# Kernel optimization log

Measured on AMD Instinct MI355X. Metric: run time of the kernel, lower is better.

## Reference

```python
import jax, jax.numpy as jnp
import numpy as np

N_USER = 20000
N_ITEM = 20000
N = N_USER + N_ITEM          # total nodes
D = 128                      # n_hid (= in_feats = out_feats)
H = 4                        # GAT heads
L = 2                        # n_layers
M = 8                        # mem_size (hypernet bottleneck)
T = 5                        # num_rels in MemoryLayer
E_UI = 40000                 # user->item bipartite edges
E_T = 16000                  # homogeneous edges per relation type (grouped)
EPS = 1e-5


def _layer_norm(x, w, b):
    mu = x.mean(-1, keepdims=True)
    var = ((x - mu) ** 2).mean(-1, keepdims=True)
    return (x - mu) * jax.lax.rsqrt(var + EPS) * w + b


def _gat(h_src, h_dst, src_idx, dst_idx, n_dst, W, al, ar, bias):
    """DGL GATConv (shared fc, eval-mode dropout=identity, elu activation)."""
    fs = (h_src @ W.T).reshape(-1, H, D)          # [Ns, H, D]
    fd = (h_dst @ W.T).reshape(-1, H, D)          # [Nd, H, D]
    el = (fs * al).sum(-1)                        # [Ns, H]
    er = (fd * ar).sum(-1)                        # [Nd, H]
    e = jax.nn.leaky_relu(el[src_idx] + er[dst_idx], 0.2)   # [E, H]
    emax = jax.ops.segment_max(e, dst_idx, num_segments=n_dst)
    ex = jnp.exp(e - emax[dst_idx])
    denom = jax.ops.segment_sum(ex, dst_idx, num_segments=n_dst)
    a = ex / denom[dst_idx]                       # edge softmax per dst
    rst = jax.ops.segment_sum(a[:, :, None] * fs[src_idx], dst_idx, num_segments=n_dst)
    return jax.nn.elu(rst + bias.reshape(1, H, D))           # [Nd, H, D]


def _memory_layer(feat, edge_src, edge_dst, Wc, bc, Ww, nWc, nbc, nWw, h_bias, ln_w, ln_b):
    # edges grouped by relation type: edge_src/edge_dst are [T, E_T]
    hs = feat[edge_src]                           # [T, Et, D]
    hd = feat[edge_dst]                           # [T, Et, D]
    # per-edge hypernetwork: coef = LeakyReLU(Linear(dst)); w = Ww(coef); msg = w @ src
    coef = jax.nn.leaky_relu(jnp.einsum('ted,tmd->tem', hd, Wc) + bc[:, None, :], 0.2)
    tmp = jnp.einsum('tei,tmoi->temo', hs, Ww)    # [T, Et, M, D] -- M-bottleneck path
    msg = jnp.einsum('tem,temo->teo', coef, tmp)  # [T, Et, D]
    flat_dst = edge_dst.reshape(-1)
    s = jax.ops.segment_sum(msg.reshape(-1, D), flat_dst, num_segments=N)
    cnt = jax.ops.segment_sum(jnp.ones((flat_dst.shape[0],), feat.dtype), flat_dst, num_segments=N)
    agg = s / jnp.maximum(cnt, 1.0)[:, None]      # fn.mean (0 for isolated nodes)
    rep = _layer_norm(agg, ln_w, ln_b) + h_bias
    # self-loop node_ME(feat, feat)
    ncoef = jax.nn.leaky_relu(feat @ nWc.T + nbc, 0.2)       # [N, M]
    ntmp = jnp.einsum('ni,moi->nmo', feat, nWw)              # [N, M, D]
    rep = rep + jnp.einsum('nm,nmo->no', ncoef, ntmp)
    return jax.nn.leaky_relu(rep, 0.2)            # dropout = identity (eval)


def setup_inputs() -> dict:
    key = jax.random.key(0)
    ks = jax.random.split(key, 16)
    s = 0.05
    return {
        "embedding": jax.random.normal(ks[0], (N, D), jnp.float32),
        "gat_fc_W": jax.random.normal(ks[1], (L, 2, H * D, D), jnp.float32) * s,
        "gat_attn_l": jax.random.normal(ks[2], (L, 2, H, D), jnp.float32) * s,
        "gat_attn_r": jax.random.normal(ks[3], (L, 2, H, D), jnp.float32) * s,
        "gat_bias": jnp.zeros((L, 2, H * D), jnp.float32),
        "proj_W": jax.random.normal(ks[4], (L, 2, D, H * D), jnp.float32) * s,
        "proj_b": jnp.zeros((L, 2, D), jnp.float32),
        "mem_rel_Wc": jax.random.normal(ks[5], (L, T, M, D), jnp.float32) * s,
        "mem_rel_bc": jnp.zeros((L, T, M), jnp.float32),
        "mem_rel_Ww": jax.random.normal(ks[6], (L, T, M, D, D), jnp.float32) * s,
        "mem_node_Wc": jax.random.normal(ks[7], (L, M, D), jnp.float32) * s,
        "mem_node_bc": jnp.zeros((L, M), jnp.float32),
        "mem_node_Ww": jax.random.normal(ks[8], (L, M, D, D), jnp.float32) * s,
        "mem_h_bias": jnp.zeros((L, D), jnp.float32),
        "mem_ln_w": jnp.ones((L, D), jnp.float32),
        "mem_ln_b": jnp.zeros((L, D), jnp.float32),
        "final_ln_w": jnp.ones(((L + 1) * D,), jnp.float32),
        "final_ln_b": jnp.zeros(((L + 1) * D,), jnp.float32),
        "src_u": jax.random.randint(ks[9], (E_UI,), 0, N_USER, jnp.int32),
        "dst_i": jax.random.randint(ks[10], (E_UI,), 0, N_ITEM, jnp.int32),
        "edge_src": jax.random.randint(ks[11], (T, E_T), 0, N, jnp.int32),
        "edge_dst": jax.random.randint(ks[12], (T, E_T), 0, N, jnp.int32),
    }


def reference(embedding, gat_fc_W, gat_attn_l, gat_attn_r, gat_bias, proj_W, proj_b,
              mem_rel_Wc, mem_rel_bc, mem_rel_Ww, mem_node_Wc, mem_node_bc, mem_node_Ww,
              mem_h_bias, mem_ln_w, mem_ln_b, final_ln_w, final_ln_b,
              src_u, dst_i, edge_src, edge_dst):
    features = embedding
    all_emb = [features]
    for l in range(L):
        hu, hi = features[:N_USER], features[N_USER:]
        # relation 0: item -> user (dst = user)
        gu = _gat(hi, hu, dst_i, src_u, N_USER,
                  gat_fc_W[l, 0], gat_attn_l[l, 0], gat_attn_r[l, 0], gat_bias[l, 0])
        ru = jax.nn.elu(gu.reshape(N_USER, H * D) @ proj_W[l, 0].T + proj_b[l, 0])
        # relation 1: user -> item (dst = item)
        gi = _gat(hu, hi, src_u, dst_i, N_ITEM,
                  gat_fc_W[l, 1], gat_attn_l[l, 1], gat_attn_r[l, 1], gat_bias[l, 1])
        ri = jnp.asarray(jax.nn.elu(gi.reshape(N_ITEM, H * D) @ proj_W[l, 1].T + proj_b[l, 1]))
        trans = jnp.concatenate([ru, ri], axis=0)             # [N, D]
        mem = _memory_layer(all_emb[-1], edge_src, edge_dst,
                            mem_rel_Wc[l], mem_rel_bc[l], mem_rel_Ww[l],
                            mem_node_Wc[l], mem_node_bc[l], mem_node_Ww[l],
                            mem_h_bias[l], mem_ln_w[l], mem_ln_b[l])
        features = mem + trans
        all_emb.append(features)
    return _layer_norm(jnp.concatenate(all_emb, axis=1), final_ln_w, final_ln_b)
```

## Files before the change

### kernel.cpp

```cpp
#include <hip/hip_runtime.h>
#include <hip/hip_bf16.h>
#include <math.h>

typedef __hip_bfloat16 bf16;

#define NUSER 20000
#define NITEM 20000
#define NTOT  40000
#define DD    128
#define HH    4
#define TT    5
#define MMEM  8
#define EUI   40000
#define ET    16000

#define MP_N  40064
#define MP_H  20096

typedef __attribute__((ext_vector_type(8))) short short8;
typedef __attribute__((ext_vector_type(4))) float f32x4;

__device__ __forceinline__ void gload16(const bf16* g, bf16* l){
  __builtin_amdgcn_global_load_lds(
      (const __attribute__((address_space(1))) unsigned int*)g,
      (__attribute__((address_space(3))) unsigned int*)l, 16, 0, 0);
}

__device__ __forceinline__ int stage_cg(int lane){
  return (((lane&3) ^ ((lane>>2)&3) ^ (lane>>4)) << 3);
}
__device__ __forceinline__ int read_pc8(int lm, int lq){
  return ((lq ^ (lm&3) ^ ((lm>>2)&3)) << 3);
}

__global__ __launch_bounds__(256) void k_mfma_gemm(
    const bf16* __restrict__ A, const bf16* __restrict__ B,
    const float* __restrict__ bias, float* __restrict__ C,
    long Astr, long Bstr, long biasStr, long Cstr,
    int ldc, int M, int K, int act, int accum)
{
  A += (size_t)blockIdx.z*Astr; B += (size_t)blockIdx.z*Bstr;
  if (bias) bias += (size_t)blockIdx.z*biasStr;
  C += (size_t)blockIdx.z*Cstr;
  __shared__ bf16 As[128*32];
  __shared__ bf16 Bs[128*32];
  int tid = threadIdx.x;
  int wave = tid >> 6, lane = tid & 63;
  int r0 = blockIdx.x * 128, c0 = blockIdx.y * 128;
  int wm = (wave >> 1) * 64, wn = (wave & 1) * 64;
  f32x4 acc[4][4];
  #pragma unroll
  for (int i=0;i<4;i++)
    #pragma unroll
    for (int j=0;j<4;j++) acc[i][j] = (f32x4){0.f,0.f,0.f,0.f};

  int rq = lane >> 2;
  int cg = stage_cg(lane);
  const bf16* Ag = A + (size_t)(r0 + wave*32 + rq)*K + cg;
  const bf16* Bg = B + (size_t)(c0 + wave*32 + rq)*K + cg;
  bf16* AsW = As + wave*32*32;
  bf16* BsW = Bs + wave*32*32;
  int lm = lane & 15, lq = lane >> 4;
  int pc8 = read_pc8(lm, lq);
  const bf16* Ard = As + (wm + lm)*32 + pc8;
  const bf16* Brd = Bs + (wn + lm)*32 + pc8;

  for (int k0 = 0; k0 < K; k0 += 32){
    gload16(Ag + k0,            AsW);
    gload16(Ag + 16*K + k0,     AsW + 16*32);
    gload16(Bg + k0,            BsW);
    gload16(Bg + 16*K + k0,     BsW + 16*32);
    __syncthreads();
    short8 af[4], bfv[4];
    #pragma unroll
    for (int i=0;i<4;i++) af[i]  = *(const short8*)(Ard + i*16*32);
    #pragma unroll
    for (int j=0;j<4;j++) bfv[j] = *(const short8*)(Brd + j*16*32);
    #pragma unroll
    for (int i=0;i<4;i++)
      #pragma unroll
      for (int j=0;j<4;j++)
        acc[i][j] = __builtin_amdgcn_mfma_f32_16x16x32_bf16(af[i], bfv[j], acc[i][j], 0, 0, 0);
    __syncthreads();
  }
  #pragma unroll
  for (int i=0;i<4;i++){
    #pragma unroll
    for (int j=0;j<4;j++){
      int c = c0 + wn + j*16 + lm;
      #pragma unroll
      for (int rg=0; rg<4; rg++){
        int r = r0 + wm + i*16 + lq*4 + rg;
        if (r < M){
          float v = acc[i][j][rg];
          if (bias) v += bias[c];
          if (act==1) v = v>0.f ? v : expm1f(v);
          float* cp = &C[(size_t)r*ldc + c];
          if (accum) *cp += v; else *cp = v;
        }
      }
    }
  }
}

__global__ __launch_bounds__(256) void k_memgemm(
    const float* __restrict__ feat, const int* __restrict__ src,
    const float* __restrict__ coef, const bf16* __restrict__ B,
    float* __restrict__ C,
    long srcStr, long coefStr, long Bstr, long Cstr,
    int Mvalid, int accum)
{
  __shared__ bf16 Af[128*136];
  __shared__ float cfS[128*8];
  __shared__ bf16 Bs[2][128*32];
  int t = blockIdx.y;
  const int*   srcT  = src ? src + (size_t)t*srcStr : nullptr;
  const float* coefT = coef + (size_t)t*coefStr;
  const bf16*  Bt    = B + (size_t)t*Bstr;
  float*       Ct    = C + (size_t)t*Cstr;
  int tid = threadIdx.x, wave = tid >> 6, lane = tid & 63;
  int r0 = blockIdx.x * 128;

  {
    int rL = tid >> 1, hf = tid & 1;
    int r = r0 + rL;
    bool valid = r < Mvalid;
    int s = valid ? (srcT ? srcT[r] : r) : 0;
    const float4* fp = (const float4*)(feat + (size_t)s*128 + hf*64);
    bf16* ap = Af + rL*136 + hf*64;
    #pragma unroll
    for (int q=0;q<16;q++){
      float4 v = fp[q];
      __hip_bfloat162 p0 = __float22bfloat162_rn(make_float2(v.x, v.y));
      __hip_bfloat162 p1 = __float22bfloat162_rn(make_float2(v.z, v.w));
      *(__hip_bfloat162*)(ap + q*4)     = p0;
      *(__hip_bfloat162*)(ap + q*4 + 2) = p1;
    }
    if (hf == 0){
      float4 c0v, c1v;
      if (valid){
        c0v = *(const float4*)(coefT + (size_t)r*8);
        c1v = *(const float4*)(coefT + (size_t)r*8 + 4);
      } else { c0v = make_float4(0.f,0.f,0.f,0.f); c1v = c0v; }
      *(float4*)(cfS + rL*8)     = c0v;
      *(float4*)(cfS + rL*8 + 4) = c1v;
    }
  }

  int rq = lane >> 2;
  int cg = stage_cg(lane);
  const bf16* Bg0 = Bt + (size_t)(wave*32 + rq)*1024 + cg;
  const bf16* Bg1 = Bt + (size_t)(wave*32 + 16 + rq)*1024 + cg;

  int wm = (wave >> 1) * 64, wn = (wave & 1) * 64;
  int lm = lane & 15, lq = lane >> 4;
  int pc8 = read_pc8(lm, lq);

  f32x4 acc[4][4];
  #pragma unroll
  for (int i=0;i<4;i++)
    #pragma unroll
    for (int j=0;j<4;j++) acc[i][j] = (f32x4){0.f,0.f,0.f,0.f};

  {
    bf16* d = Bs[0] + wave*1024;
    gload16(Bg0, d);
    gload16(Bg1, d + 512);
  }
  __syncthreads();

  int buf = 0;
  for (int m = 0; m < 8; m++){
    float cfr[4];
    #pragma unroll
    for (int i=0;i<4;i++) cfr[i] = cfS[(wm + i*16 + lm)*8 + m];
    #pragma unroll
    for (int ic = 0; ic < 4; ic++){
      int kk = m*4 + ic;
      if (kk + 1 < 32){
        int k1 = (kk + 1) * 32;
        bf16* d = Bs[buf^1] + wave*1024;
        gload16(Bg0 + k1, d);
        gload16(Bg1 + k1, d + 512);
      }
      short8 af[4], bfv[4];
      #pragma unroll
      for (int i=0;i<4;i++){
        short8 raw = *(const short8*)(Af + (size_t)(wm + i*16 + lm)*136 + ic*32 + lq*8);
        union { short8 s; unsigned u[4]; } U, V;
        U.s = raw;
        float c = cfr[i];
        #pragma unroll
        for (int p=0;p<4;p++){
          float lo = __uint_as_float(U.u[p] << 16) * c;
          float hi = __uint_as_float(U.u[p] & 0xffff0000u) * c;
          __hip_bfloat162 pk = __float22bfloat162_rn(make_float2(lo, hi));
          V.u[p] = *(unsigned*)&pk;
        }
        af[i] = V.s;
      }
      #pragma unroll
      for (int j=0;j<4;j++)
        bfv[j] = *(const short8*)(Bs[buf] + (wn + lm + j*16)*32 + pc8);
      #pragma unroll
      for (int i=0;i<4;i++)
        #pragma unroll
        for (int j=0;j<4;j++)
          acc[i][j] = __builtin_amdgcn_mfma_f32_16x16x32_bf16(af[i], bfv[j], acc[i][j], 0, 0, 0);
      __syncthreads();
      buf ^= 1;
    }
  }
  #pragma unroll
  for (int i=0;i<4;i++){
    #pragma unroll
    for (int j=0;j<4;j++){
      int c = wn + j*16 + lm;
      #pragma unroll
      for (int rg=0; rg<4; rg++){
        int r = r0 + wm + i*16 + lq*4 + rg;
        if (r < Mvalid){
          float* cp = &Ct[(size_t)r*128 + c];
          if (accum) *cp += acc[i][j][rg]; else *cp = acc[i][j][rg];
        }
      }
    }
  }
}

__global__ void k_f2b(const float* __restrict__ in, bf16* __restrict__ o, int nv, int nt){
  int i = blockIdx.x*256 + threadIdx.x;
  if (i < nt) o[i] = __float2bfloat16(i < nv ? in[i] : 0.f);
}

__global__ void k_repack(const float* __restrict__ in, bf16* __restrict__ o){
  int s = blockIdx.y;
  int g = blockIdx.x*256 + threadIdx.x;
  int m = g >> 14, od = (g >> 7) & 127, i = g & 127;
  o[(size_t)s*131072 + (size_t)od*1024 + m*128 + i] = __float2bfloat16(in[(size_t)s*131072 + g]);
}

__global__ void k_rstb(const float* __restrict__ rst, const float* __restrict__ gb,
                       bf16* __restrict__ o){
  int r = blockIdx.x, t = threadIdx.x;
  int k = t*4;
  bf16* op = o + (size_t)r*512 + k;
  if (r < 20000){
    const float* ip = rst + (size_t)r*512 + k;
    #pragma unroll
    for (int q=0;q<4;q++){
      float v = ip[q] + gb[k+q];
      v = v>0.f ? v : expm1f(v);
      op[q] = __float2bfloat16(v);
    }
  } else {
    #pragma unroll
    for (int q=0;q<4;q++) op[q] = __float2bfloat16(0.f);
  }
}

__global__ void k_attn(const float* __restrict__ F, const float* __restrict__ al,
                       const float* __restrict__ ar, float* __restrict__ el, float* __restrict__ er){
  int n = blockIdx.x, lane = threadIdx.x;
  const float* row = F + (size_t)n*512;
  #pragma unroll
  for (int h=0;h<HH;h++){
    float x1 = row[h*128+lane], x2 = row[h*128+64+lane];
    float vl = x1*al[h*128+lane] + x2*al[h*128+64+lane];
    float vr = x1*ar[h*128+lane] + x2*ar[h*128+64+lane];
    #pragma unroll
    for (int off=32;off;off>>=1){ vl += __shfl_xor(vl,off); vr += __shfl_xor(vr,off); }
    if (lane==0){ el[n*4+h]=vl; er[n*4+h]=vr; }
  }
}

__global__ void k_hist(const int* __restrict__ dIdx, int* __restrict__ cnt, int E){
  int e = blockIdx.x*256+threadIdx.x;
  if (e<E) atomicAdd(&cnt[dIdx[e]], 1);
}

__global__ __launch_bounds__(1024) void k_scan(const int* __restrict__ in,
                                               int* __restrict__ out, int n){
  __shared__ int wsum[16];
  __shared__ int carry;
  int tidx = threadIdx.x, lane = tidx & 63, w = tidx >> 6;
  if (tidx == 0) carry = 0;
  __syncthreads();
  for (int base = 0; base < n; base += 1024){
    int i = base + tidx;
    int v = (i < n) ? in[i] : 0;
    int x = v;
    #pragma unroll
    for (int off = 1; off < 64; off <<= 1){
      int t = __shfl_up(x, off);
      if (lane >= off) x += t;
    }
    if (lane == 63) wsum[w] = x;
    __syncthreads();
    if (w == 0 && lane < 16){
      int t = wsum[lane];
      #pragma unroll
      for (int off=1; off<16; off<<=1){
        int u = __shfl_up(t, off, 16);
        if (lane >= off) t += u;
      }
      wsum[lane] = t;
    }
    __syncthreads();
    int woff = (w == 0) ? 0 : wsum[w-1];
    int excl = carry + woff + x - v;
    if (i < n) out[i] = excl;
    __syncthreads();
    if (tidx == 1023) carry = carry + wsum[15];
    __syncthreads();
  }
  if (tidx == 0) out[n] = carry;
}

__global__ void k_csr_scatter(const int* __restrict__ sIdx, const int* __restrict__ dIdx,
                              int sOff, const int* __restrict__ rowptr,
                              int* __restrict__ cursor, int* __restrict__ col, int E){
  int e = blockIdx.x*256+threadIdx.x; if (e>=E) return;
  int d = dIdx[e];
  int pos = rowptr[d] + atomicAdd(&cursor[d], 1);
  col[pos] = sIdx[e] + sOff;
}

__global__ void k_csr_scatter_eid(const int* __restrict__ dIdx, const int* __restrict__ rowptr,
                                  int* __restrict__ cursor, int* __restrict__ col, int E){
  int e = blockIdx.x*256+threadIdx.x; if (e>=E) return;
  int d = dIdx[e];
  int pos = rowptr[d] + atomicAdd(&cursor[d], 1);
  col[pos] = e;
}

__global__ __launch_bounds__(64) void k_gat_gather(
    const int* __restrict__ rowptr, const int* __restrict__ col,
    const float* __restrict__ el, const float* __restrict__ er,
    const float* __restrict__ F, float* __restrict__ rst,
    int dOff, int n_dst)
{
  int dl = blockIdx.x;
  int dn = dl + dOff;
  int lane = threadIdx.x;
  int h = lane >> 4;
  int off = (lane & 15) << 3;
  float erh = er[dn*4 + h];
  float m = -INFINITY, den = 0.f;
  float acc[8];
  #pragma unroll
  for (int i=0;i<8;i++) acc[i]=0.f;
  int jb = rowptr[dl], je = rowptr[dl+1];
  for (int j=jb; j<je; j++){
    int s = col[j];
    float e = el[s*4+h] + erh;
    e = e > 0.f ? e : 0.2f*e;
    float mn = fmaxf(m, e);
    float sc = __expf(m - mn);
    float wj = __expf(e - mn);
    den = den*sc + wj;
    m = mn;
    const float4* fp = (const float4*)(F + (size_t)s*512 + h*128 + off);
    float4 f0 = fp[0], f1 = fp[1];
    acc[0]=acc[0]*sc + wj*f0.x; acc[1]=acc[1]*sc + wj*f0.y;
    acc[2]=acc[2]*sc + wj*f0.z; acc[3]=acc[3]*sc + wj*f0.w;
    acc[4]=acc[4]*sc + wj*f1.x; acc[5]=acc[5]*sc + wj*f1.y;
    acc[6]=acc[6]*sc + wj*f1.z; acc[7]=acc[7]*sc + wj*f1.w;
  }
  float inv = den > 0.f ? 1.f/den : 0.f;
  float* rp = rst + (size_t)dl*512 + h*128 + off;
  ((float4*)rp)[0] = make_float4(acc[0]*inv, acc[1]*inv, acc[2]*inv, acc[3]*inv);
  ((float4*)rp)[1] = make_float4(acc[4]*inv, acc[5]*inv, acc[6]*inv, acc[7]*inv);
}

__global__ void k_coef(const float* __restrict__ feat, const int* __restrict__ idx,
                       const float* __restrict__ Wc, const float* __restrict__ bc,
                       float* __restrict__ outc, int cnt){
  int t = blockIdx.y;
  __shared__ float wS[MMEM*DD];
  __shared__ float bS[MMEM];
  for (int i=threadIdx.x;i<MMEM*DD;i+=128) wS[i] = Wc[(size_t)t*MMEM*DD + i];
  if (threadIdx.x < MMEM) bS[threadIdx.x] = bc[t*MMEM + threadIdx.x];
  __syncthreads();
  int e = blockIdx.x*128 + threadIdx.x; if (e >= cnt) return;
  int node = idx ? idx[(size_t)t*cnt + e] : e;
  float acc[MMEM];
  #pragma unroll
  for (int m=0;m<MMEM;m++) acc[m]=bS[m];
  const float* fr = feat + (size_t)node*DD;
  for (int d2=0; d2<DD; d2++){
    float v = fr[d2];
    #pragma unroll
    for (int m=0;m<MMEM;m++) acc[m] = fmaf(v, wS[m*DD+d2], acc[m]);
  }
  float* op = outc + ((size_t)t*cnt + e)*MMEM;
  #pragma unroll
  for (int m=0;m<MMEM;m++){ float v=acc[m]; op[m] = v>0.f ? v : 0.2f*v; }
}

__global__ void k_mem_gather(const int* __restrict__ rpT, const int* __restrict__ colT,
                             const float* __restrict__ msg, float* __restrict__ sAgg){
  int n = blockIdx.x*4 + (threadIdx.x >> 6);
  if (n >= NTOT) return;
  int lane = threadIdx.x & 63;
  int jb = rpT[n], je = rpT[n+1];
  float a0=0.f, a1=0.f;
  for (int j=jb;j<je;j++){
    const float* mp = msg + (size_t)colT[j]*128;
    a0 += mp[lane]; a1 += mp[lane+64];
  }
  sAgg[(size_t)n*128+lane] = a0;
  sAgg[(size_t)n*128+64+lane] = a1;
}

__global__ void k_memln(const float* __restrict__ s, const int* __restrict__ rpT,
                        const float* __restrict__ lw, const float* __restrict__ lb,
                        const float* __restrict__ hb, float* __restrict__ outp){
  int n = blockIdx.x, lane = threadIdx.x;
  float c = fmaxf((float)(rpT[n+1]-rpT[n]), 1.f);
  float x1 = s[(size_t)n*128+lane]/c, x2 = s[(size_t)n*128+64+lane]/c;
  float t = x1+x2;
  #pragma unroll
  for (int off=32;off;off>>=1) t += __shfl_xor(t,off);
  float mu = t * (1.f/128.f);
  float d1=x1-mu, d2=x2-mu;
  float v = d1*d1+d2*d2;
  #pragma unroll
  for (int off=32;off;off>>=1) v += __shfl_xor(v,off);
  float r = rsqrtf(v*(1.f/128.f) + 1e-5f);
  outp[(size_t)n*128+lane]    = d1*r*lw[lane]    + lb[lane]    + hb[lane];
  outp[(size_t)n*128+64+lane] = d2*r*lw[64+lane] + lb[64+lane] + hb[64+lane];
}

__global__ void k_final_feat(const float* __restrict__ mo, const float* __restrict__ tr,
                             float* __restrict__ o, int n){
  int i = blockIdx.x*256+threadIdx.x; if (i>=n) return;
  float v = mo[i]; v = v>0.f ? v : 0.2f*v;
  o[i] = v + tr[i];
}

__global__ void k_final_ln(const float* __restrict__ emb, const float* __restrict__ f1,
                           const float* __restrict__ f2, const float* __restrict__ w,
                           const float* __restrict__ b, float* __restrict__ out){
  int n = blockIdx.x, t = threadIdx.x;
  __shared__ float red[4];
  float x0 = emb[(size_t)n*128+t];
  float x1 = f1[(size_t)n*128+t];
  float x2 = f2[(size_t)n*128+t];
  float s = x0+x1+x2;
  #pragma unroll
  for (int off=32;off;off>>=1) s += __shfl_xor(s,off);
  if ((t&63)==0) red[t>>6] = s;
  __syncthreads();
  float mu = (red[0]+red[1]) * (1.f/384.f);
  float d0=x0-mu, d1=x1-mu, d2=x2-mu;
  float v = d0*d0+d1*d1+d2*d2;
  #pragma unroll
  for (int off=32;off;off>>=1) v += __shfl_xor(v,off);
  if ((t&63)==0) red[2+(t>>6)] = v;
  __syncthreads();
  float var = (red[2]+red[3]) * (1.f/384.f);
  float r = rsqrtf(var + 1e-5f);
  size_t o = (size_t)n*384;
  out[o+t]     = d0*r*w[t]     + b[t];
  out[o+128+t] = d1*r*w[128+t] + b[128+t];
  out[o+256+t] = d2*r*w[256+t] + b[256+t];
}

extern "C" void kernel_launch(void* const* d_in, const int* in_sizes, int n_in,
                              void* d_out, int out_size, void* d_ws, size_t ws_size,
                              hipStream_t stream)
{
  const float* emb   = (const float*)d_in[0];
  const float* fcW   = (const float*)d_in[1];
  const float* attl  = (const float*)d_in[2];
  const float* attr  = (const float*)d_in[3];
  const float* gbias = (const float*)d_in[4];
  const float* projW = (const float*)d_in[5];
  const float* projB = (const float*)d_in[6];
  const float* relWc = (const float*)d_in[7];
  const float* relbc = (const float*)d_in[8];
  const float* relWw = (const float*)d_in[9];
  const float* nodWc = (const float*)d_in[10];
  const float* nodbc = (const float*)d_in[11];
  const float* nodWw = (const float*)d_in[12];
  const float* hbias = (const float*)d_in[13];
  const float* mlnw  = (const float*)d_in[14];
  const float* mlnb  = (const float*)d_in[15];
  const float* flnw  = (const float*)d_in[16];
  const float* flnb  = (const float*)d_in[17];
  const int*  srcU  = (const int*)d_in[18];
  const int*  dstI  = (const int*)d_in[19];
  const int*  eSrc  = (const int*)d_in[20];
  const int*  eDst  = (const int*)d_in[21];
  float* out = (float*)d_out;

  char* wp = (char*)d_ws;
  auto alloc = [&](size_t bytes)->void* {
    void* p = (void*)wp; wp += (bytes + 511) & ~(size_t)511; return p;
  };
  float* feat1 = (float*)alloc((size_t)NTOT*DD*4);
  float* feat2 = (float*)alloc((size_t)NTOT*DD*4);
  float* Fbuf  = (float*)alloc((size_t)NTOT*512*4);
  float* rst   = (float*)alloc((size_t)(NTOT+256)*512*4);
  float* trans = (float*)alloc((size_t)NTOT*DD*4);
  float* elF   = (float*)alloc((size_t)NTOT*4*4);
  float* erF   = (float*)alloc((size_t)NTOT*4*4);
  int* rpA  = (int*)alloc((size_t)(NUSER+1)*4);
  int* colA = (int*)alloc((size_t)EUI*4);
  int* rpB  = (int*)alloc((size_t)(NITEM+1)*4);
  int* colB = (int*)alloc((size_t)EUI*4);
  int* icnt = (int*)alloc((size_t)20000*4);
  int* icur = (int*)alloc((size_t)20000*4);
  int* rpT  = (int*)alloc((size_t)(NTOT+1)*4);
  int* colT = (int*)alloc((size_t)TT*ET*4);
  int* cntT = (int*)alloc((size_t)NTOT*4);
  int* icurT= (int*)alloc((size_t)NTOT*4);
  bf16* featb  = (bf16*)alloc((size_t)MP_N*DD*2);
  bf16* fcWb   = (bf16*)alloc((size_t)4*512*DD*2);
  bf16* projWb = (bf16*)alloc((size_t)4*DD*512*2);
  bf16* relWwb = (bf16*)alloc((size_t)10*DD*1024*2);
  bf16* nodWwb = (bf16*)alloc((size_t)2*DD*1024*2);
  bf16* rstb0 = (bf16*)(rst + (size_t)20000*512);
  bf16* rstb1 = rstb0 + (size_t)MP_H*512;
  float* sAgg   = rst;
  float* memO   = rst + (size_t)NTOT*DD;
  float* msgB   = Fbuf;
  float* coefB  = Fbuf + (size_t)TT*ET*128;
  float* ncoefB = coefB + (size_t)TT*ET*8;

  k_f2b<<<dim3((4*512*DD+255)/256),256,0,stream>>>(fcW, fcWb, 4*512*DD, 4*512*DD);
  k_f2b<<<dim3((4*DD*512+255)/256),256,0,stream>>>(projW, projWb, 4*DD*512, 4*DD*512);
  k_repack<<<dim3(512,10),256,0,stream>>>(relWw, relWwb);
  k_repack<<<dim3(512,2),256,0,stream>>>(nodWw, nodWwb);

  hipMemsetAsync(icnt, 0, 20000*4, stream);
  hipMemsetAsync(icur, 0, 20000*4, stream);
  k_hist<<<dim3((EUI+255)/256),256,0,stream>>>(srcU, icnt, EUI);
  k_scan<<<dim3(1),1024,0,stream>>>(icnt, rpA, NUSER);
  k_csr_scatter<<<dim3((EUI+255)/256),256,0,stream>>>(dstI, srcU, NUSER, rpA, icur, colA, EUI);
  hipMemsetAsync(icnt, 0, 20000*4, stream);
  hipMemsetAsync(icur, 0, 20000*4, stream);
  k_hist<<<dim3((EUI+255)/256),256,0,stream>>>(dstI, icnt, EUI);
  k_scan<<<dim3(1),1024,0,stream>>>(icnt, rpB, NITEM);
  k_csr_scatter<<<dim3((EUI+255)/256),256,0,stream>>>(srcU, dstI, 0, rpB, icur, colB, EUI);
  hipMemsetAsync(cntT, 0, NTOT*4, stream);
  hipMemsetAsync(icurT, 0, NTOT*4, stream);
  k_hist<<<dim3((TT*ET+255)/256),256,0,stream>>>(eDst, cntT, TT*ET);
  k_scan<<<dim3(1),1024,0,stream>>>(cntT, rpT, NTOT);
  k_csr_scatter_eid<<<dim3((TT*ET+255)/256),256,0,stream>>>(eDst, rpT, icurT, colT, TT*ET);

  const float* feats[3] = {emb, feat1, feat2};
  for (int l=0; l<2; l++){
    const float* fin  = feats[l];
    float* fout = (float*)feats[l+1];

    k_f2b<<<dim3((MP_N*DD+255)/256),256,0,stream>>>(fin, featb, NTOT*DD, MP_N*DD);

    for (int d=0; d<2; d++){
      k_mfma_gemm<<<dim3(MP_N/128, 4, 1),256,0,stream>>>(
          featb, fcWb + (size_t)(l*2+d)*512*DD, nullptr, Fbuf,
          0,0,0,0, 512, NTOT, DD, 0, 0);
      k_attn<<<dim3(NTOT),64,0,stream>>>(Fbuf,
          attl+(size_t)(l*2+d)*512, attr+(size_t)(l*2+d)*512, elF, erF);
      int dOff = (d==0) ? 0 : NUSER;
      const int* rp  = (d==0) ? rpA : rpB;
      const int* col = (d==0) ? colA : colB;
      k_gat_gather<<<dim3(20000),64,0,stream>>>(rp, col, elF, erF, Fbuf, rst, dOff, 20000);
      k_rstb<<<dim3(MP_H),128,0,stream>>>(rst, gbias+(size_t)(l*2+d)*512,
                                          (d==0) ? rstb0 : rstb1);
    }
    k_mfma_gemm<<<dim3(MP_H/128, 1, 2),256,0,stream>>>(
        rstb0, projWb + (size_t)(l*2)*DD*512, projB + (size_t)(l*2)*DD, trans,
        (long)MP_H*512, (long)DD*512, (long)DD, (long)20000*DD,
        DD, 20000, 512, 1, 0);

    k_coef<<<dim3((ET+127)/128, TT),128,0,stream>>>(fin, eDst,
        relWc+(size_t)l*TT*MMEM*DD, relbc+(size_t)l*TT*MMEM, coefB, ET);
    k_memgemm<<<dim3(ET/128, TT),256,0,stream>>>(
        fin, eSrc, coefB, relWwb + (size_t)l*TT*DD*1024, msgB,
        (long)ET, (long)ET*8, (long)DD*1024, (long)ET*128, ET, 0);
    k_mem_gather<<<dim3(NTOT/4),256,0,stream>>>(rpT, colT, msgB, sAgg);
    k_memln<<<dim3(NTOT),64,0,stream>>>(sAgg, rpT, mlnw+(size_t)l*DD, mlnb+(size_t)l*DD,
                                        hbias+(size_t)l*DD, memO);
    k_coef<<<dim3((NTOT+127)/128, 1),128,0,stream>>>(fin, nullptr,
        nodWc+(size_t)l*MMEM*DD, nodbc+(size_t)l*MMEM, ncoefB, NTOT);
    k_memgemm<<<dim3(MP_N/128, 1),256,0,stream>>>(
        fin, nullptr, ncoefB, nodWwb + (size_t)l*DD*1024, memO,
        0, 0, 0, 0, NTOT, 1);
    k_final_feat<<<dim3((NTOT*DD+255)/256),256,0,stream>>>(memO, trans, fout, NTOT*DD);
  }

  k_final_ln<<<dim3(NTOT),128,0,stream>>>(emb, feat1, feat2, flnw, flnb, out);
}
```

Measured before the change: 1.053 ms.

## Fuse attention scores into FC GEMM, store bf16 intermediates, restructure memgemm

```diff
diff --git a/kernel.cpp b/kernel.cpp
--- a/kernel.cpp
+++ b/kernel.cpp
@@ -25,6 +25,8 @@
       (const __attribute__((address_space(1))) unsigned int*)g,
       (__attribute__((address_space(3))) unsigned int*)l, 16, 0, 0);
 }
+__device__ __forceinline__ float bu2f_lo(unsigned u){ return __uint_as_float(u << 16); }
+__device__ __forceinline__ float bu2f_hi(unsigned u){ return __uint_as_float(u & 0xffff0000u); }
 
 __device__ __forceinline__ int stage_cg(int lane){
   return (((lane&3) ^ ((lane>>2)&3) ^ (lane>>4)) << 3);
@@ -103,48 +105,151 @@
   }
 }
 
+__global__ __launch_bounds__(256) void k_fc_gemm(
+    const bf16* __restrict__ A, const bf16* __restrict__ B,
+    bf16* __restrict__ Fb, const float* __restrict__ al, const float* __restrict__ ar,
+    float* __restrict__ el, float* __restrict__ er, int M)
+{
+  __shared__ bf16 As[128*32];
+  __shared__ bf16 Bs[128*32];
+  __shared__ float redE[2][2][128];
+  int tid = threadIdx.x;
+  int wave = tid >> 6, lane = tid & 63;
+  int h = blockIdx.y;
+  int r0 = blockIdx.x * 128;
+  int wm = (wave >> 1) * 64, wn = (wave & 1) * 64;
+  f32x4 acc[4][4];
+  #pragma unroll
+  for (int i=0;i<4;i++)
+    #pragma unroll
+    for (int j=0;j<4;j++) acc[i][j] = (f32x4){0.f,0.f,0.f,0.f};
+
+  int rq = lane >> 2;
+  int cg = stage_cg(lane);
+  const bf16* Ag = A + (size_t)(r0 + wave*32 + rq)*128 + cg;
+  const bf16* Bg = B + (size_t)(h*128 + wave*32 + rq)*128 + cg;
+  bf16* AsW = As + wave*32*32;
+  bf16* BsW = Bs + wave*32*32;
+  int lm = lane & 15, lq = lane >> 4;
+  int pc8 = read_pc8(lm, lq);
+  const bf16* Ard = As + (wm + lm)*32 + pc8;
+  const bf16* Brd = Bs + (wn + lm)*32 + pc8;
+
+  for (int k0 = 0; k0 < 128; k0 += 32){
+    gload16(Ag + k0,             AsW);
+    gload16(Ag + 16*128 + k0,    AsW + 16*32);
+    gload16(Bg + k0,             BsW);
+    gload16(Bg + 16*128 + k0,    BsW + 16*32);
+    __syncthreads();
+    short8 af[4], bfv[4];
+    #pragma unroll
+    for (int i=0;i<4;i++) af[i]  = *(const short8*)(Ard + i*16*32);
+    #pragma unroll
+    for (int j=0;j<4;j++) bfv[j] = *(const short8*)(Brd + j*16*32);
+    #pragma unroll
+    for (int i=0;i<4;i++)
+      #pragma unroll
+      for (int j=0;j<4;j++)
+        acc[i][j] = __builtin_amdgcn_mfma_f32_16x16x32_bf16(af[i], bfv[j], acc[i][j], 0, 0, 0);
+    __syncthreads();
+  }
+  float alv[4], arv[4];
+  #pragma unroll
+  for (int j=0;j<4;j++){
+    int c = h*128 + wn + j*16 + lm;
+    alv[j] = al[c]; arv[j] = ar[c];
+  }
+  int wnh = wave & 1;
+  #pragma unroll
+  for (int i=0;i<4;i++){
+    #pragma unroll
+    for (int rg=0; rg<4; rg++){
+      float se = 0.f, sr = 0.f;
+      #pragma unroll
+      for (int j=0;j<4;j++){
+        float v = acc[i][j][rg];
+        se = fmaf(v, alv[j], se);
+        sr = fmaf(v, arv[j], sr);
+      }
+      #pragma unroll
+      for (int msk=1; msk<16; msk<<=1){
+        se += __shfl_xor(se, msk);
+        sr += __shfl_xor(sr, msk);
+      }
+      if (lm == 0){
+        int rl = wm + i*16 + lq*4 + rg;
+        redE[0][wnh][rl] = se;
+        redE[1][wnh][rl] = sr;
+      }
+    }
+  }
+  #pragma unroll
+  for (int i=0;i<4;i++){
+    #pragma unroll
+    for (int j=0;j<4;j++){
+      int c = h*128 + wn + j*16 + lm;
+      #pragma unroll
+      for (int rg=0; rg<4; rg++){
+        int r = r0 + wm + i*16 + lq*4 + rg;
+        if (r < M) Fb[(size_t)r*512 + c] = __float2bfloat16(acc[i][j][rg]);
+      }
+    }
+  }
+  __syncthreads();
+  if (tid < 128){
+    int r = r0 + tid;
+    if (r < M) el[(size_t)r*4 + h] = redE[0][0][tid] + redE[0][1][tid];
+  } else {
+    int t2 = tid - 128;
+    int r = r0 + t2;
+    if (r < M) er[(size_t)r*4 + h] = redE[1][0][t2] + redE[1][1][t2];
+  }
+}
+
 __global__ __launch_bounds__(256) void k_memgemm(
     const float* __restrict__ feat, const int* __restrict__ src,
     const float* __restrict__ coef, const bf16* __restrict__ B,
-    float* __restrict__ C,
-    long srcStr, long coefStr, long Bstr, long Cstr,
-    int Mvalid, int accum)
+    float* __restrict__ C, bf16* __restrict__ Cb,
+    const float* __restrict__ trans, float* __restrict__ fout,
+    long srcStr, long coefStr, long Bstr, long CbStr,
+    int Mvalid, int mode)
 {
-  __shared__ bf16 Af[128*136];
-  __shared__ float cfS[128*8];
+  __shared__ bf16 Af[64*144];
+  __shared__ float cfS[8*64];
   __shared__ bf16 Bs[2][128*32];
   int t = blockIdx.y;
   const int*   srcT  = src ? src + (size_t)t*srcStr : nullptr;
   const float* coefT = coef + (size_t)t*coefStr;
   const bf16*  Bt    = B + (size_t)t*Bstr;
-  float*       Ct    = C + (size_t)t*Cstr;
   int tid = threadIdx.x, wave = tid >> 6, lane = tid & 63;
-  int r0 = blockIdx.x * 128;
+  int r0 = blockIdx.x * 64;
 
   {
-    int rL = tid >> 1, hf = tid & 1;
+    int rL = tid >> 2, seg = tid & 3;
     int r = r0 + rL;
     bool valid = r < Mvalid;
     int s = valid ? (srcT ? srcT[r] : r) : 0;
-    const float4* fp = (const float4*)(feat + (size_t)s*128 + hf*64);
-    bf16* ap = Af + rL*136 + hf*64;
-    #pragma unroll
-    for (int q=0;q<16;q++){
-      float4 v = fp[q];
-      __hip_bfloat162 p0 = __float22bfloat162_rn(make_float2(v.x, v.y));
-      __hip_bfloat162 p1 = __float22bfloat162_rn(make_float2(v.z, v.w));
+    const float4* fp = (const float4*)(feat + (size_t)s*128 + seg*32);
+    bf16* ap = Af + rL*144 + seg*32;
+    #pragma unroll
+    for (int q=0;q<8;q+=2){
+      float4 v0 = fp[q], v1 = fp[q+1];
+      __hip_bfloat162 p0 = __float22bfloat162_rn(make_float2(v0.x, v0.y));
+      __hip_bfloat162 p1 = __float22bfloat162_rn(make_float2(v0.z, v0.w));
+      __hip_bfloat162 p2 = __float22bfloat162_rn(make_float2(v1.x, v1.y));
+      __hip_bfloat162 p3 = __float22bfloat162_rn(make_float2(v1.z, v1.w));
       *(__hip_bfloat162*)(ap + q*4)     = p0;
       *(__hip_bfloat162*)(ap + q*4 + 2) = p1;
-    }
-    if (hf == 0){
-      float4 c0v, c1v;
-      if (valid){
-        c0v = *(const float4*)(coefT + (size_t)r*8);
-        c1v = *(const float4*)(coefT + (size_t)r*8 + 4);
-      } else { c0v = make_float4(0.f,0.f,0.f,0.f); c1v = c0v; }
-      *(float4*)(cfS + rL*8)     = c0v;
-      *(float4*)(cfS + rL*8 + 4) = c1v;
-    }
+      *(__hip_bfloat162*)(ap + q*4 + 4) = p2;
+      *(__hip_bfloat162*)(ap + q*4 + 6) = p3;
+    }
+  }
+  if (tid < 64){
+    int r = r0 + tid;
+    bool valid = r < Mvalid;
+    #pragma unroll
+    for (int m=0;m<8;m++)
+      cfS[m*64 + tid] = valid ? coefT[(size_t)r*8 + m] : 0.f;
   }
 
   int rq = lane >> 2;
@@ -152,15 +257,15 @@
   const bf16* Bg0 = Bt + (size_t)(wave*32 + rq)*1024 + cg;
   const bf16* Bg1 = Bt + (size_t)(wave*32 + 16 + rq)*1024 + cg;
 
-  int wm = (wave >> 1) * 64, wn = (wave & 1) * 64;
+  int wm = (wave >> 1) * 32, wn = (wave & 1) * 64;
   int lm = lane & 15, lq = lane >> 4;
   int pc8 = read_pc8(lm, lq);
 
-  f32x4 acc[4][4];
-  #pragma unroll
-  for (int i=0;i<4;i++)
-    #pragma unroll
-    for (int j=0;j<4;j++) acc[i][j] = (f32x4){0.f,0.f,0.f,0.f};
+  f32x4 accC[2][4];
+  #pragma unroll
+  for (int i=0;i<2;i++)
+    #pragma unroll
+    for (int j=0;j<4;j++) accC[i][j] = (f32x4){0.f,0.f,0.f,0.f};
 
   {
     bf16* d = Bs[0] + wave*1024;
@@ -170,10 +275,9 @@
   __syncthreads();
 
   int buf = 0;
+  #pragma unroll
   for (int m = 0; m < 8; m++){
-    float cfr[4];
-    #pragma unroll
-    for (int i=0;i<4;i++) cfr[i] = cfS[(wm + i*16 + lm)*8 + m];
+    f32x4 accM[2][4];
     #pragma unroll
     for (int ic = 0; ic < 4; ic++){
       int kk = m*4 + ic;
@@ -183,36 +287,42 @@
         gload16(Bg0 + k1, d);
         gload16(Bg1 + k1, d + 512);
       }
-      short8 af[4], bfv[4];
-      #pragma unroll
-      for (int i=0;i<4;i++){
-        short8 raw = *(const short8*)(Af + (size_t)(wm + i*16 + lm)*136 + ic*32 + lq*8);
-        union { short8 s; unsigned u[4]; } U, V;
-        U.s = raw;
-        float c = cfr[i];
-        #pragma unroll
-        for (int p=0;p<4;p++){
-          float lo = __uint_as_float(U.u[p] << 16) * c;
-          float hi = __uint_as_float(U.u[p] & 0xffff0000u) * c;
-          __hip_bfloat162 pk = __float22bfloat162_rn(make_float2(lo, hi));
-          V.u[p] = *(unsigned*)&pk;
-        }
-        af[i] = V.s;
-      }
+      short8 af[2], bfv[4];
+      #pragma unroll
+      for (int i=0;i<2;i++)
+        af[i] = *(const short8*)(Af + (size_t)(wm + i*16 + lm)*144 + ic*32 + lq*8);
       #pragma unroll
       for (int j=0;j<4;j++)
         bfv[j] = *(const short8*)(Bs[buf] + (wn + lm + j*16)*32 + pc8);
-      #pragma unroll
-      for (int i=0;i<4;i++)
+      if (ic == 0){
         #pragma unroll
-        for (int j=0;j<4;j++)
-          acc[i][j] = __builtin_amdgcn_mfma_f32_16x16x32_bf16(af[i], bfv[j], acc[i][j], 0, 0, 0);
+        for (int i=0;i<2;i++)
+          #pragma unroll
+          for (int j=0;j<4;j++)
+            accM[i][j] = __builtin_amdgcn_mfma_f32_16x16x32_bf16(af[i], bfv[j],
+                             (f32x4){0.f,0.f,0.f,0.f}, 0, 0, 0);
+      } else {
+        #pragma unroll
+        for (int i=0;i<2;i++)
+          #pragma unroll
+          for (int j=0;j<4;j++)
+            accM[i][j] = __builtin_amdgcn_mfma_f32_16x16x32_bf16(af[i], bfv[j], accM[i][j], 0, 0, 0);
+      }
       __syncthreads();
       buf ^= 1;
     }
-  }
-  #pragma unroll
-  for (int i=0;i<4;i++){
+    #pragma unroll
+    for (int i=0;i<2;i++){
+      f32x4 cf4 = *(const f32x4*)(cfS + m*64 + wm + i*16 + lq*4);
+      #pragma unroll
+      for (int j=0;j<4;j++)
+        #pragma unroll
+        for (int rg=0; rg<4; rg++)
+          accC[i][j][rg] = fmaf(cf4[rg], accM[i][j][rg], accC[i][j][rg]);
+    }
+  }
+  #pragma unroll
+  for (int i=0;i<2;i++){
     #pragma unroll
     for (int j=0;j<4;j++){
       int c = wn + j*16 + lm;
@@ -220,8 +330,14 @@
       for (int rg=0; rg<4; rg++){
         int r = r0 + wm + i*16 + lq*4 + rg;
         if (r < Mvalid){
-          float* cp = &Ct[(size_t)r*128 + c];
-          if (accum) *cp += acc[i][j][rg]; else *cp = acc[i][j][rg];
+          float v = accC[i][j][rg];
+          if (mode == 0){
+            Cb[(size_t)t*CbStr + (size_t)r*128 + c] = __float2bfloat16(v);
+          } else {
+            float x = C[(size_t)r*128 + c] + v;
+            x = x>0.f ? x : 0.2f*x;
+            fout[(size_t)r*128 + c] = x + trans[(size_t)r*128 + c];
+          }
         }
       }
     }
@@ -238,40 +354,6 @@
   int g = blockIdx.x*256 + threadIdx.x;
   int m = g >> 14, od = (g >> 7) & 127, i = g & 127;
   o[(size_t)s*131072 + (size_t)od*1024 + m*128 + i] = __float2bfloat16(in[(size_t)s*131072 + g]);
-}
-
-__global__ void k_rstb(const float* __restrict__ rst, const float* __restrict__ gb,
-                       bf16* __restrict__ o){
-  int r = blockIdx.x, t = threadIdx.x;
-  int k = t*4;
-  bf16* op = o + (size_t)r*512 + k;
-  if (r < 20000){
-    const float* ip = rst + (size_t)r*512 + k;
-    #pragma unroll
-    for (int q=0;q<4;q++){
-      float v = ip[q] + gb[k+q];
-      v = v>0.f ? v : expm1f(v);
-      op[q] = __float2bfloat16(v);
-    }
-  } else {
-    #pragma unroll
-    for (int q=0;q<4;q++) op[q] = __float2bfloat16(0.f);
-  }
-}
-
-__global__ void k_attn(const float* __restrict__ F, const float* __restrict__ al,
-                       const float* __restrict__ ar, float* __restrict__ el, float* __restrict__ er){
-  int n = blockIdx.x, lane = threadIdx.x;
-  const float* row = F + (size_t)n*512;
-  #pragma unroll
-  for (int h=0;h<HH;h++){
-    float x1 = row[h*128+lane], x2 = row[h*128+64+lane];
-    float vl = x1*al[h*128+lane] + x2*al[h*128+64+lane];
-    float vr = x1*ar[h*128+lane] + x2*ar[h*128+64+lane];
-    #pragma unroll
-    for (int off=32;off;off>>=1){ vl += __shfl_xor(vl,off); vr += __shfl_xor(vr,off); }
-    if (lane==0){ el[n*4+h]=vl; er[n*4+h]=vr; }
-  }
 }
 
 __global__ void k_hist(const int* __restrict__ dIdx, int* __restrict__ cnt, int E){
@@ -337,15 +419,14 @@
 __global__ __launch_bounds__(64) void k_gat_gather(
     const int* __restrict__ rowptr, const int* __restrict__ col,
     const float* __restrict__ el, const float* __restrict__ er,
-    const float* __restrict__ F, float* __restrict__ rst,
-    int dOff, int n_dst)
+    const bf16* __restrict__ Fb, const float* __restrict__ gb,
+    bf16* __restrict__ rstb, int dOff)
 {
   int dl = blockIdx.x;
-  int dn = dl + dOff;
   int lane = threadIdx.x;
   int h = lane >> 4;
   int off = (lane & 15) << 3;
-  float erh = er[dn*4 + h];
+  float erh = er[(size_t)(dl + dOff)*4 + h];
   float m = -INFINITY, den = 0.f;
   float acc[8];
   #pragma unroll
@@ -353,24 +434,31 @@
   int jb = rowptr[dl], je = rowptr[dl+1];
   for (int j=jb; j<je; j++){
     int s = col[j];
-    float e = el[s*4+h] + erh;
+    float e = el[(size_t)s*4+h] + erh;
     e = e > 0.f ? e : 0.2f*e;
     float mn = fmaxf(m, e);
     float sc = __expf(m - mn);
     float wj = __expf(e - mn);
     den = den*sc + wj;
     m = mn;
-    const float4* fp = (const float4*)(F + (size_t)s*512 + h*128 + off);
-    float4 f0 = fp[0], f1 = fp[1];
-    acc[0]=acc[0]*sc + wj*f0.x; acc[1]=acc[1]*sc + wj*f0.y;
-    acc[2]=acc[2]*sc + wj*f0.z; acc[3]=acc[3]*sc + wj*f0.w;
-    acc[4]=acc[4]*sc + wj*f1.x; acc[5]=acc[5]*sc + wj*f1.y;
-    acc[6]=acc[6]*sc + wj*f1.z; acc[7]=acc[7]*sc + wj*f1.w;
+    uint4 u = *(const uint4*)(Fb + (size_t)s*512 + h*128 + off);
+    acc[0]=acc[0]*sc + wj*bu2f_lo(u.x); acc[1]=acc[1]*sc + wj*bu2f_hi(u.x);
+    acc[2]=acc[2]*sc + wj*bu2f_lo(u.y); acc[3]=acc[3]*sc + wj*bu2f_hi(u.y);
+    acc[4]=acc[4]*sc + wj*bu2f_lo(u.z); acc[5]=acc[5]*sc + wj*bu2f_hi(u.z);
+    acc[6]=acc[6]*sc + wj*bu2f_lo(u.w); acc[7]=acc[7]*sc + wj*bu2f_hi(u.w);
   }
   float inv = den > 0.f ? 1.f/den : 0.f;
-  float* rp = rst + (size_t)dl*512 + h*128 + off;
-  ((float4*)rp)[0] = make_float4(acc[0]*inv, acc[1]*inv, acc[2]*inv, acc[3]*inv);
-  ((float4*)rp)[1] = make_float4(acc[4]*inv, acc[5]*inv, acc[6]*inv, acc[7]*inv);
+  int cb = h*128 + off;
+  float x[8];
+  #pragma unroll
+  for (int q=0;q<8;q++){
+    float v = acc[q]*inv + gb[cb+q];
+    x[q] = v>0.f ? v : expm1f(v);
+  }
+  union { uint4 u; __hip_bfloat162 p[4]; } O;
+  #pragma unroll
+  for (int q=0;q<4;q++) O.p[q] = __float22bfloat162_rn(make_float2(x[2*q], x[2*q+1]));
+  *(uint4*)(rstb + (size_t)dl*512 + cb) = O.u;
 }
 
 __global__ void k_coef(const float* __restrict__ feat, const int* __restrict__ idx,
@@ -399,18 +487,17 @@
 }
 
 __global__ void k_mem_gather(const int* __restrict__ rpT, const int* __restrict__ colT,
-                             const float* __restrict__ msg, float* __restrict__ sAgg){
+                             const bf16* __restrict__ msg, float* __restrict__ sAgg){
   int n = blockIdx.x*4 + (threadIdx.x >> 6);
   if (n >= NTOT) return;
   int lane = threadIdx.x & 63;
   int jb = rpT[n], je = rpT[n+1];
   float a0=0.f, a1=0.f;
   for (int j=jb;j<je;j++){
-    const float* mp = msg + (size_t)colT[j]*128;
-    a0 += mp[lane]; a1 += mp[lane+64];
-  }
-  sAgg[(size_t)n*128+lane] = a0;
-  sAgg[(size_t)n*128+64+lane] = a1;
+    unsigned u = ((const unsigned*)(msg + (size_t)colT[j]*128))[lane];
+    a0 += bu2f_lo(u); a1 += bu2f_hi(u);
+  }
+  *(float2*)(sAgg + (size_t)n*128 + lane*2) = make_float2(a0, a1);
 }
 
 __global__ void k_memln(const float* __restrict__ s, const int* __restrict__ rpT,
@@ -430,13 +517,6 @@
   float r = rsqrtf(v*(1.f/128.f) + 1e-5f);
   outp[(size_t)n*128+lane]    = d1*r*lw[lane]    + lb[lane]    + hb[lane];
   outp[(size_t)n*128+64+lane] = d2*r*lw[64+lane] + lb[64+lane] + hb[64+lane];
-}
-
-__global__ void k_final_feat(const float* __restrict__ mo, const float* __restrict__ tr,
-                             float* __restrict__ o, int n){
-  int i = blockIdx.x*256+threadIdx.x; if (i>=n) return;
-  float v = mo[i]; v = v>0.f ? v : 0.2f*v;
-  o[i] = v + tr[i];
 }
 
 __global__ void k_final_ln(const float* __restrict__ emb, const float* __restrict__ f1,
@@ -502,7 +582,8 @@
   float* feat1 = (float*)alloc((size_t)NTOT*DD*4);
   float* feat2 = (float*)alloc((size_t)NTOT*DD*4);
   float* Fbuf  = (float*)alloc((size_t)NTOT*512*4);
-  float* rst   = (float*)alloc((size_t)(NTOT+256)*512*4);
+  float* rst   = (float*)alloc((size_t)NTOT*DD*2*4);
+  bf16*  rstb0 = (bf16*)alloc((size_t)2*MP_H*512*2);
   float* trans = (float*)alloc((size_t)NTOT*DD*4);
   float* elF   = (float*)alloc((size_t)NTOT*4*4);
   float* erF   = (float*)alloc((size_t)NTOT*4*4);
@@ -521,18 +602,20 @@
   bf16* projWb = (bf16*)alloc((size_t)4*DD*512*2);
   bf16* relWwb = (bf16*)alloc((size_t)10*DD*1024*2);
   bf16* nodWwb = (bf16*)alloc((size_t)2*DD*1024*2);
-  bf16* rstb0 = (bf16*)(rst + (size_t)20000*512);
-  bf16* rstb1 = rstb0 + (size_t)MP_H*512;
+  bf16*  Fb     = (bf16*)Fbuf;
+  bf16*  msgBb  = (bf16*)((char*)Fbuf + (size_t)NTOT*512*2);
+  float* coefB  = (float*)((char*)msgBb + (size_t)TT*ET*128*2);
+  float* ncoefB = coefB + (size_t)TT*ET*8;
+  bf16*  rstb1  = rstb0 + (size_t)MP_H*512;
   float* sAgg   = rst;
   float* memO   = rst + (size_t)NTOT*DD;
-  float* msgB   = Fbuf;
-  float* coefB  = Fbuf + (size_t)TT*ET*128;
-  float* ncoefB = coefB + (size_t)TT*ET*8;
 
   k_f2b<<<dim3((4*512*DD+255)/256),256,0,stream>>>(fcW, fcWb, 4*512*DD, 4*512*DD);
   k_f2b<<<dim3((4*DD*512+255)/256),256,0,stream>>>(projW, projWb, 4*DD*512, 4*DD*512);
   k_repack<<<dim3(512,10),256,0,stream>>>(relWw, relWwb);
   k_repack<<<dim3(512,2),256,0,stream>>>(nodWw, nodWwb);
+  hipMemsetAsync(rstb0 + (size_t)20000*512, 0, (size_t)(MP_H-20000)*512*2, stream);
+  hipMemsetAsync(rstb1 + (size_t)20000*512, 0, (size_t)(MP_H-20000)*512*2, stream);
 
   hipMemsetAsync(icnt, 0, 20000*4, stream);
   hipMemsetAsync(icur, 0, 20000*4, stream);
@@ -558,17 +641,14 @@
     k_f2b<<<dim3((MP_N*DD+255)/256),256,0,stream>>>(fin, featb, NTOT*DD, MP_N*DD);
 
     for (int d=0; d<2; d++){
-      k_mfma_gemm<<<dim3(MP_N/128, 4, 1),256,0,stream>>>(
-          featb, fcWb + (size_t)(l*2+d)*512*DD, nullptr, Fbuf,
-          0,0,0,0, 512, NTOT, DD, 0, 0);
-      k_attn<<<dim3(NTOT),64,0,stream>>>(Fbuf,
-          attl+(size_t)(l*2+d)*512, attr+(size_t)(l*2+d)*512, elF, erF);
+      k_fc_gemm<<<dim3(MP_N/128, 4),256,0,stream>>>(
+          featb, fcWb + (size_t)(l*2+d)*512*DD, Fb,
+          attl+(size_t)(l*2+d)*512, attr+(size_t)(l*2+d)*512, elF, erF, NTOT);
       int dOff = (d==0) ? 0 : NUSER;
       const int* rp  = (d==0) ? rpA : rpB;
       const int* col = (d==0) ? colA : colB;
-      k_gat_gather<<<dim3(20000),64,0,stream>>>(rp, col, elF, erF, Fbuf, rst, dOff, 20000);
-      k_rstb<<<dim3(MP_H),128,0,stream>>>(rst, gbias+(size_t)(l*2+d)*512,
-                                          (d==0) ? rstb0 : rstb1);
+      k_gat_gather<<<dim3(20000),64,0,stream>>>(rp, col, elF, erF, Fb,
+          gbias+(size_t)(l*2+d)*512, (d==0) ? rstb0 : rstb1, dOff);
     }
     k_mfma_gemm<<<dim3(MP_H/128, 1, 2),256,0,stream>>>(
         rstb0, projWb + (size_t)(l*2)*DD*512, projB + (size_t)(l*2)*DD, trans,
@@ -577,18 +657,19 @@
 
     k_coef<<<dim3((ET+127)/128, TT),128,0,stream>>>(fin, eDst,
         relWc+(size_t)l*TT*MMEM*DD, relbc+(size_t)l*TT*MMEM, coefB, ET);
-    k_memgemm<<<dim3(ET/128, TT),256,0,stream>>>(
-        fin, eSrc, coefB, relWwb + (size_t)l*TT*DD*1024, msgB,
+    k_memgemm<<<dim3(ET/64, TT),256,0,stream>>>(
+        fin, eSrc, coefB, relWwb + (size_t)l*TT*DD*1024,
+        nullptr, msgBb, nullptr, nullptr,
         (long)ET, (long)ET*8, (long)DD*1024, (long)ET*128, ET, 0);
-    k_mem_gather<<<dim3(NTOT/4),256,0,stream>>>(rpT, colT, msgB, sAgg);
+    k_mem_gather<<<dim3(NTOT/4),256,0,stream>>>(rpT, colT, msgBb, sAgg);
     k_memln<<<dim3(NTOT),64,0,stream>>>(sAgg, rpT, mlnw+(size_t)l*DD, mlnb+(size_t)l*DD,
                                         hbias+(size_t)l*DD, memO);
     k_coef<<<dim3((NTOT+127)/128, 1),128,0,stream>>>(fin, nullptr,
         nodWc+(size_t)l*MMEM*DD, nodbc+(size_t)l*MMEM, ncoefB, NTOT);
-    k_memgemm<<<dim3(MP_N/128, 1),256,0,stream>>>(
-        fin, nullptr, ncoefB, nodWwb + (size_t)l*DD*1024, memO,
-        0, 0, 0, 0, NTOT, 1);
-    k_final_feat<<<dim3((NTOT*DD+255)/256),256,0,stream>>>(memO, trans, fout, NTOT*DD);
+    k_memgemm<<<dim3(MP_N/64, 1),256,0,stream>>>(
+        fin, nullptr, ncoefB, nodWwb + (size_t)l*DD*1024,
+        memO, nullptr, trans, fout,
+        0, 0, 0, 0, NTOT, 2);
   }
 
   k_final_ln<<<dim3(NTOT),128,0,stream>>>(emb, feat1, feat2, flnw, flnb, out);
```

Result: faster. 950.8 us (-9.7%).
